# Optimization experiments

Measured on AMD Instinct MI355X. Metric: run time of the kernel, lower is better.

Reference implementation:

```python
import jax, jax.numpy as jnp
import numpy as np

B, M, L, IN_C, MID_C, OUT_C = 1, 128, 256, 256, 32, 128


def setup_inputs() -> dict:
    key = jax.random.key(0)
    k_x, k_proj, k_final = jax.random.split(key, 3)
    return {
        "x1d": jax.random.normal(k_x, (B, M, L, IN_C), dtype=jnp.float32),
        "norm_w": jnp.ones((IN_C,), dtype=jnp.float32),
        "norm_b": jnp.zeros((IN_C,), dtype=jnp.float32),
        "proj_w": jax.random.normal(k_proj, (2 * MID_C, IN_C), dtype=jnp.float32) * 0.02,
        "proj_b": jnp.zeros((2 * MID_C,), dtype=jnp.float32),
        "final_w": jax.random.normal(k_final, (OUT_C, MID_C * MID_C), dtype=jnp.float32) * 0.02,
        "final_b": jnp.zeros((OUT_C,), dtype=jnp.float32),
    }


def reference(x1d, norm_w, norm_b, proj_w, proj_b, final_w, final_b):
    # LayerNorm over channel dim
    mu = jnp.mean(x1d, axis=-1, keepdims=True)
    var = jnp.mean(jnp.square(x1d - mu), axis=-1, keepdims=True)
    x = (x1d - mu) * jax.lax.rsqrt(var + 1e-5) * norm_w + norm_b

    mid_c = proj_w.shape[0] // 2
    # Linear -> (b, m, L, 2*mid_c); view (..., mid_c, 2); chunk & squeeze:
    # i = interleaved even channels, j = interleaved odd channels
    p = jnp.einsum('bmlc,dc->bmld', x, proj_w) + proj_b
    p = p.reshape(*p.shape[:-1], mid_c, 2)
    i, j = p[..., 0], p[..., 1]          # each (b, m, L, mid_c)

    m = x1d.shape[1]
    # Outer product mean over the MSA (m) dimension -> (b, L, L, mid_c, mid_c)
    x2d = jnp.einsum('bmix,bmjy->bijxy', i, j) / m

    b, li, lj = x2d.shape[0], x2d.shape[1], x2d.shape[2]
    flat = x2d.reshape(b, li, lj, mid_c * mid_c)
    out = jnp.einsum('bijf,of->bijo', flat, final_w) + final_b
    return out
```

## Files before the change

kernel.cpp:

```cpp
#include <hip/hip_runtime.h>
#include <hip/hip_bf16.h>

#define DEVINL __device__ __forceinline__

typedef float  f32x4_t  __attribute__((ext_vector_type(4)));
typedef float  f32x16_t __attribute__((ext_vector_type(16)));
typedef short  bf16x8_t __attribute__((ext_vector_type(8)));

#define MFMA16(a,b,c) __builtin_amdgcn_mfma_f32_16x16x32_bf16((a),(b),(c),0,0,0)
#define MFMA32(a,b,c) __builtin_amdgcn_mfma_f32_32x32x16_bf16((a),(b),(c),0,0,0)

DEVINL unsigned short f2bf(float f) {
  union { float f; unsigned u; } v; v.f = f;
  unsigned r = v.u + 0x7fffu + ((v.u >> 16) & 1u);
  return (unsigned short)(r >> 16);
}

DEVINL unsigned pk2bf(float lo, float hi) {
  union { __hip_bfloat162 h2; unsigned u; } v;
  v.h2 = __float22bfloat162_rn(make_float2(lo, hi));
  return v.u;
}


__global__ __launch_bounds__(256) void kA(const float* __restrict__ x,
                                          const float* __restrict__ nw,
                                          const float* __restrict__ nb,
                                          const float* __restrict__ pw,
                                          const float* __restrict__ pb,
                                          const float* __restrict__ fw,
                                          unsigned short* __restrict__ Wb,
                                          unsigned short* __restrict__ Ig,
                                          unsigned short* __restrict__ Jg) {
  if (blockIdx.x >= 1024) {
    int T = (blockIdx.x - 1024) * 256 + threadIdx.x;
    int o     = T >> 8;
    int kpos0 = (T & 255) * 4;
    int y  = kpos0 >> 5;
    int x0 = kpos0 & 31;
    const float* fo = fw + o * 1024 + y;
    ushort4 u;
    u.x = f2bf(fo[(x0 + 0) * 32]);
    u.y = f2bf(fo[(x0 + 1) * 32]);
    u.z = f2bf(fo[(x0 + 2) * 32]);
    u.w = f2bf(fo[(x0 + 3) * 32]);
    size_t off = (size_t)((o >> 5) * 64 + (kpos0 >> 4)) * 512 + (o & 31) * 16
               + ((kpos0 >> 3) & 1) * 8 + (kpos0 & 7);
    *(ushort4*)&Wb[off] = u;
    return;
  }
  __shared__ unsigned short xnl[32 * 264];
  __shared__ unsigned short pwl[64 * 264];
  __shared__ unsigned short ep[64 * 36];
  const int tid  = threadIdx.x;
  const int wv   = tid >> 6;
  const int lane = tid & 63;
  const int q    = lane >> 4;
  const int ln16 = lane & 15;
  const int l    = blockIdx.x & 255;
  const int m0   = (blockIdx.x >> 8) * 32;

  const float4* xs = (const float4*)x;
  float4 v[8];
#pragma unroll
  for (int i = 0; i < 8; i++) {
    int row = m0 + i * 4 + wv;
    v[i] = xs[row * 16384 + l * 64 + lane];
  }
  float4 nw4 = ((const float4*)nw)[lane];
  float4 nb4 = ((const float4*)nb)[lane];

#pragma unroll
  for (int i = 0; i < 8; i++) {
    float s  = v[i].x + v[i].y + v[i].z + v[i].w;
    float ss = v[i].x * v[i].x + v[i].y * v[i].y + v[i].z * v[i].z + v[i].w * v[i].w;
#pragma unroll
    for (int off = 32; off > 0; off >>= 1) {
      s  += __shfl_xor(s, off);
      ss += __shfl_xor(ss, off);
    }
    float mu  = s * (1.0f / 256.0f);
    float var = ss * (1.0f / 256.0f) - mu * mu;
    float rs  = rsqrtf(var + 1e-5f);
    ushort4 u;
    u.x = f2bf((v[i].x - mu) * rs * nw4.x + nb4.x);
    u.y = f2bf((v[i].y - mu) * rs * nw4.y + nb4.y);
    u.z = f2bf((v[i].z - mu) * rs * nw4.z + nb4.z);
    u.w = f2bf((v[i].w - mu) * rs * nw4.w + nb4.w);
    *(ushort4*)&xnl[(i * 4 + wv) * 264 + lane * 4] = u;
  }

  const float4* ps = (const float4*)pw;
#pragma unroll
  for (int i = 0; i < 16; i++) {
    float4 w4 = ps[i * 256 + tid];
    ushort4 u;
    u.x = f2bf(w4.x); u.y = f2bf(w4.y); u.z = f2bf(w4.z); u.w = f2bf(w4.w);
    *(ushort4*)&pwl[(i * 4 + wv) * 264 + lane * 4] = u;
  }
  __syncthreads();

  const int rt = wv & 1;
  const int db = (wv >> 1) * 32;
  f32x4_t acc[2] = {{0.f, 0.f, 0.f, 0.f}, {0.f, 0.f, 0.f, 0.f}};
#pragma unroll
  for (int kc = 0; kc < 8; kc++) {
    bf16x8_t a  = *(const bf16x8_t*)&xnl[(rt * 16 + ln16) * 264 + kc * 32 + q * 8];
    bf16x8_t b0 = *(const bf16x8_t*)&pwl[(db + ln16) * 264 + kc * 32 + q * 8];
    bf16x8_t b1 = *(const bf16x8_t*)&pwl[(db + 16 + ln16) * 264 + kc * 32 + q * 8];
    acc[0] = MFMA16(a, b0, acc[0]);
    acc[1] = MFMA16(a, b1, acc[1]);
  }

#pragma unroll
  for (int t2 = 0; t2 < 2; t2++) {
    int d = db + t2 * 16 + ln16;
    float bias  = pb[d];
    float scale = (d & 1) ? 1.0f : (1.0f / 128.0f);
#pragma unroll
    for (int r = 0; r < 4; r++) {
      int mloc = rt * 16 + q * 4 + r;
      ep[d * 36 + mloc] = f2bf((acc[t2][r] + bias) * scale);
    }
  }
  __syncthreads();

  const int h  = tid >> 3;
  const int m4 = tid & 7;
  const size_t off = (size_t)(l * 8 + (m0 >> 4) + (m4 >> 2)) * 512 + h * 16 + ((m4 >> 1) & 1) * 8 + (m4 & 1) * 4;
  ushort4 vi = *(const ushort4*)&ep[(2 * h) * 36 + m4 * 4];
  *(ushort4*)&Ig[off] = vi;
  ushort4 vj = *(const ushort4*)&ep[(2 * h + 1) * 36 + m4 * 4];
  *(ushort4*)&Jg[off] = vj;
}

__global__ __launch_bounds__(512, 4) void kB(const unsigned short* __restrict__ Ig,
                                             const unsigned short* __restrict__ Jg,
                                             const unsigned short* __restrict__ Wb,
                                             const float* __restrict__ fb,
                                             float* __restrict__ out) {
  extern __shared__ unsigned short fl[];
  constexpr int P = 1048;
  const int tid  = threadIdx.x;
  const int w    = tid >> 6;
  const int lane = tid & 63;
  const int ln32 = lane & 31;
  const int h    = lane >> 5;
  const int p    = blockIdx.x >> 4;
  const int t    = blockIdx.x & 15;

  const int u  = w & 1;
  const int sq = w >> 1;
  bf16x8_t af[8];
#pragma unroll
  for (int mc = 0; mc < 8; mc++)
    af[mc] = *(const bf16x8_t*)&Ig[(size_t)((p * 2 + u) * 8 + mc) * 512 + ln32 * 16 + h * 8];

#pragma unroll
  for (int s = 0; s < 4; s++) {
    const int jl = sq * 4 + s;
    const size_t jbase = (size_t)(t * 16 + jl) * 4096 + ln32 * 16 + h * 8;
    bf16x8_t jb[8];
#pragma unroll
    for (int mc = 0; mc < 8; mc++) jb[mc] = *(const bf16x8_t*)&Jg[jbase + mc * 512];
    f32x16_t c;
#pragma unroll
    for (int i = 0; i < 16; i++) c[i] = 0.f;
#pragma unroll
    for (int mc = 0; mc < 8; mc++) c = MFMA32(af[mc], jb[mc], c);
    unsigned short* fr = &fl[(u * 16 + jl) * P];
#pragma unroll
    for (int g = 0; g < 4; g++) {
      int cp = (4 * ln32 + g) ^ (ln32 & 7);
      uint2 pv;
      pv.x = pk2bf(c[4 * g + 0], c[4 * g + 1]);
      pv.y = pk2bf(c[4 * g + 2], c[4 * g + 3]);
      *(uint2*)&fr[cp * 8 + h * 4] = pv;
    }
  }

  const int ot = w & 3;
  const int kh = w >> 2;
  const unsigned short* Wp = Wb + (size_t)(ot * 64 + kh * 32) * 512 + ln32 * 16 + h * 8;
  bf16x8_t bq[8];
  bq[0] = *(const bf16x8_t*)&Wp[0];
  bq[1] = *(const bf16x8_t*)&Wp[512];

  __syncthreads();

#pragma unroll
  for (int i = 2; i < 8; i++) bq[i] = *(const bf16x8_t*)&Wp[(size_t)i * 512];

#define LDA(kc) (*(const bf16x8_t*)&fl[ln32 * P + \
    ((((kh * 32 + (kc)) * 2 + h) ^ (((kh * 32 + (kc)) >> 1) & 7)) * 8)])

  f32x16_t o2[2];
#pragma unroll
  for (int i = 0; i < 16; i++) { o2[0][i] = 0.f; o2[1][i] = 0.f; }

  bf16x8_t aq[4];
  aq[0] = LDA(0); aq[1] = LDA(1); aq[2] = LDA(2); aq[3] = LDA(3);

#pragma unroll
  for (int kc = 0; kc < 32; kc += 2) {
    bf16x8_t ac0 = aq[kc & 3],      ac1 = aq[(kc + 1) & 3];
    bf16x8_t bc0 = bq[kc & 7],      bc1 = bq[(kc + 1) & 7];
    if (kc < 28) { aq[kc & 3] = LDA(kc + 4); aq[(kc + 1) & 3] = LDA(kc + 5); }
    if (kc < 24) {
      bq[kc & 7]       = *(const bf16x8_t*)&Wp[(size_t)(kc + 8) * 512];
      bq[(kc + 1) & 7] = *(const bf16x8_t*)&Wp[(size_t)(kc + 9) * 512];
    }
    o2[0] = MFMA32(ac0, bc0, o2[0]);
    o2[1] = MFMA32(ac1, bc1, o2[1]);
  }
#undef LDA

#pragma unroll
  for (int i = 0; i < 16; i++) o2[0][i] += o2[1][i];

  __syncthreads();
  float* red = (float*)fl;
  if (kh == 1) {
#pragma unroll
    for (int q = 0; q < 4; q++) {
      int idx = ot * 1024 + lane * 16 + ((q ^ (lane & 3)) * 4);
      *(float4*)&red[idx] = make_float4(o2[0][4 * q + 0], o2[0][4 * q + 1],
                                        o2[0][4 * q + 2], o2[0][4 * q + 3]);
    }
  }
  __syncthreads();
  if (kh == 0) {
#pragma unroll
    for (int q = 0; q < 4; q++) {
      int idx = ot * 1024 + lane * 16 + ((q ^ (lane & 3)) * 4);
      float4 rv = *(const float4*)&red[idx];
      o2[0][4 * q + 0] += rv.x; o2[0][4 * q + 1] += rv.y;
      o2[0][4 * q + 2] += rv.z; o2[0][4 * q + 3] += rv.w;
    }
    const float bias = fb[ot * 32 + ln32];
    float* ob = out + ((size_t)(p * 2) * 256 + t * 16) * 128 + ot * 32 + ln32;
#pragma unroll
    for (int r = 0; r < 16; r++) {
      int br = (r & 3) + 8 * (r >> 2) + 4 * h;
      ob[(br >> 4) * 32768 + (br & 15) * 128] = o2[0][r] + bias;
    }
  }
}

extern "C" void kernel_launch(void* const* d_in, const int* in_sizes, int n_in,
                              void* d_out, int out_size, void* d_ws, size_t ws_size,
                              hipStream_t stream) {
  const float* x1d     = (const float*)d_in[0];
  const float* norm_w  = (const float*)d_in[1];
  const float* norm_b  = (const float*)d_in[2];
  const float* proj_w  = (const float*)d_in[3];
  const float* proj_b  = (const float*)d_in[4];
  const float* final_w = (const float*)d_in[5];
  const float* final_b = (const float*)d_in[6];
  float* outp          = (float*)d_out;

  unsigned short* Wb  = (unsigned short*)d_ws;
  unsigned short* Igp = Wb + 131072;
  unsigned short* Jgp = Igp + 1048576;

  const int kb_lds = 32 * 1048 * 2;
  hipFuncSetAttribute((const void*)kB, hipFuncAttributeMaxDynamicSharedMemorySize, kb_lds);

  kA<<<1152, 256, 0, stream>>>(x1d, norm_w, norm_b, proj_w, proj_b, final_w, Wb, Igp, Jgp);
  kB<<<2048, 512, kb_lds, stream>>>(Igp, Jgp, Wb, final_b, outp);
}
```

Before: 138.8 us.

## Double kB tile to 64 output rows per 1024-thread block

```diff
diff --git a/kernel.cpp b/kernel.cpp
--- a/kernel.cpp
+++ b/kernel.cpp
@@ -134,11 +134,11 @@
   *(ushort4*)&Jg[off] = vj;
 }
 
-__global__ __launch_bounds__(512, 4) void kB(const unsigned short* __restrict__ Ig,
-                                             const unsigned short* __restrict__ Jg,
-                                             const unsigned short* __restrict__ Wb,
-                                             const float* __restrict__ fb,
-                                             float* __restrict__ out) {
+__global__ __launch_bounds__(1024, 4) void kB(const unsigned short* __restrict__ Ig,
+                                              const unsigned short* __restrict__ Jg,
+                                              const unsigned short* __restrict__ Wb,
+                                              const float* __restrict__ fb,
+                                              float* __restrict__ out) {
   extern __shared__ unsigned short fl[];
   constexpr int P = 1048;
   const int tid  = threadIdx.x;
@@ -149,101 +149,108 @@
   const int p    = blockIdx.x >> 4;
   const int t    = blockIdx.x & 15;
 
-  const int u  = w & 1;
-  const int sq = w >> 1;
-  bf16x8_t af[8];
-#pragma unroll
-  for (int mc = 0; mc < 8; mc++)
-    af[mc] = *(const bf16x8_t*)&Ig[(size_t)((p * 2 + u) * 8 + mc) * 512 + ln32 * 16 + h * 8];
-
-#pragma unroll
-  for (int s = 0; s < 4; s++) {
-    const int jl = sq * 4 + s;
-    const size_t jbase = (size_t)(t * 16 + jl) * 4096 + ln32 * 16 + h * 8;
-    bf16x8_t jb[8];
-#pragma unroll
-    for (int mc = 0; mc < 8; mc++) jb[mc] = *(const bf16x8_t*)&Jg[jbase + mc * 512];
-    f32x16_t c;
-#pragma unroll
-    for (int i = 0; i < 16; i++) c[i] = 0.f;
-#pragma unroll
-    for (int mc = 0; mc < 8; mc++) c = MFMA32(af[mc], jb[mc], c);
-    unsigned short* fr = &fl[(u * 16 + jl) * P];
-#pragma unroll
-    for (int g = 0; g < 4; g++) {
-      int cp = (4 * ln32 + g) ^ (ln32 & 7);
-      uint2 pv;
-      pv.x = pk2bf(c[4 * g + 0], c[4 * g + 1]);
-      pv.y = pk2bf(c[4 * g + 2], c[4 * g + 3]);
-      *(uint2*)&fr[cp * 8 + h * 4] = pv;
+  {
+    const int il = w & 3;
+    const int sq = w >> 2;
+    bf16x8_t af[8];
+#pragma unroll
+    for (int mc = 0; mc < 8; mc++)
+      af[mc] = *(const bf16x8_t*)&Ig[(size_t)((p * 4 + il) * 8 + mc) * 512 + ln32 * 16 + h * 8];
+
+#pragma unroll
+    for (int s = 0; s < 4; s++) {
+      const int jl = sq * 4 + s;
+      const size_t jbase = (size_t)(t * 16 + jl) * 4096 + ln32 * 16 + h * 8;
+      bf16x8_t jb[8];
+#pragma unroll
+      for (int mc = 0; mc < 8; mc++) jb[mc] = *(const bf16x8_t*)&Jg[jbase + mc * 512];
+      f32x16_t c;
+#pragma unroll
+      for (int i = 0; i < 16; i++) c[i] = 0.f;
+#pragma unroll
+      for (int mc = 0; mc < 8; mc++) c = MFMA32(af[mc], jb[mc], c);
+      unsigned short* fr = &fl[(il * 16 + jl) * P];
+#pragma unroll
+      for (int g = 0; g < 4; g++) {
+        int cp = (4 * ln32 + g) ^ (ln32 & 7);
+        uint2 pv;
+        pv.x = pk2bf(c[4 * g + 0], c[4 * g + 1]);
+        pv.y = pk2bf(c[4 * g + 2], c[4 * g + 3]);
+        *(uint2*)&fr[cp * 8 + h * 4] = pv;
+      }
     }
   }
 
   const int ot = w & 3;
-  const int kh = w >> 2;
-  const unsigned short* Wp = Wb + (size_t)(ot * 64 + kh * 32) * 512 + ln32 * 16 + h * 8;
-  bf16x8_t bq[8];
+  const int kq = w >> 2;
+  const unsigned short* Wp = Wb + (size_t)(ot * 64 + kq * 16) * 512 + ln32 * 16 + h * 8;
+  bf16x8_t bq[4];
   bq[0] = *(const bf16x8_t*)&Wp[0];
   bq[1] = *(const bf16x8_t*)&Wp[512];
 
   __syncthreads();
 
-#pragma unroll
-  for (int i = 2; i < 8; i++) bq[i] = *(const bf16x8_t*)&Wp[(size_t)i * 512];
-
-#define LDA(kc) (*(const bf16x8_t*)&fl[ln32 * P + \
-    ((((kh * 32 + (kc)) * 2 + h) ^ (((kh * 32 + (kc)) >> 1) & 7)) * 8)])
+  bq[2] = *(const bf16x8_t*)&Wp[2 * 512];
+  bq[3] = *(const bf16x8_t*)&Wp[3 * 512];
+
+#define LDA(rt, kc) (*(const bf16x8_t*)&fl[((rt) * 32 + ln32) * P + \
+    ((((kq * 16 + (kc)) * 2 + h) ^ (((kq * 16 + (kc)) >> 1) & 7)) * 8)])
 
   f32x16_t o2[2];
 #pragma unroll
   for (int i = 0; i < 16; i++) { o2[0][i] = 0.f; o2[1][i] = 0.f; }
 
   bf16x8_t aq[4];
-  aq[0] = LDA(0); aq[1] = LDA(1); aq[2] = LDA(2); aq[3] = LDA(3);
-
-#pragma unroll
-  for (int kc = 0; kc < 32; kc += 2) {
-    bf16x8_t ac0 = aq[kc & 3],      ac1 = aq[(kc + 1) & 3];
-    bf16x8_t bc0 = bq[kc & 7],      bc1 = bq[(kc + 1) & 7];
-    if (kc < 28) { aq[kc & 3] = LDA(kc + 4); aq[(kc + 1) & 3] = LDA(kc + 5); }
-    if (kc < 24) {
-      bq[kc & 7]       = *(const bf16x8_t*)&Wp[(size_t)(kc + 8) * 512];
-      bq[(kc + 1) & 7] = *(const bf16x8_t*)&Wp[(size_t)(kc + 9) * 512];
-    }
-    o2[0] = MFMA32(ac0, bc0, o2[0]);
-    o2[1] = MFMA32(ac1, bc1, o2[1]);
+  aq[0] = LDA(0, 0); aq[1] = LDA(1, 0);
+  aq[2] = LDA(0, 1); aq[3] = LDA(1, 1);
+
+#pragma unroll
+  for (int kc = 0; kc < 16; kc++) {
+    const int sl = (kc & 1) * 2;
+    bf16x8_t a0 = aq[sl], a1 = aq[sl + 1];
+    bf16x8_t bc = bq[kc & 3];
+    if (kc < 14) { aq[sl] = LDA(0, kc + 2); aq[sl + 1] = LDA(1, kc + 2); }
+    if (kc < 12) bq[kc & 3] = *(const bf16x8_t*)&Wp[(size_t)(kc + 4) * 512];
+    o2[0] = MFMA32(a0, bc, o2[0]);
+    o2[1] = MFMA32(a1, bc, o2[1]);
   }
 #undef LDA
 
-#pragma unroll
-  for (int i = 0; i < 16; i++) o2[0][i] += o2[1][i];
-
   __syncthreads();
   float* red = (float*)fl;
-  if (kh == 1) {
-#pragma unroll
-    for (int q = 0; q < 4; q++) {
-      int idx = ot * 1024 + lane * 16 + ((q ^ (lane & 3)) * 4);
-      *(float4*)&red[idx] = make_float4(o2[0][4 * q + 0], o2[0][4 * q + 1],
-                                        o2[0][4 * q + 2], o2[0][4 * q + 3]);
-    }
-  }
-  __syncthreads();
-  if (kh == 0) {
-#pragma unroll
-    for (int q = 0; q < 4; q++) {
-      int idx = ot * 1024 + lane * 16 + ((q ^ (lane & 3)) * 4);
-      float4 rv = *(const float4*)&red[idx];
-      o2[0][4 * q + 0] += rv.x; o2[0][4 * q + 1] += rv.y;
-      o2[0][4 * q + 2] += rv.z; o2[0][4 * q + 3] += rv.w;
+  if (kq != 0) {
+    const int base = (((kq - 1) * 4 + ot) * 2) * 1024;
+#pragma unroll
+    for (int rt = 0; rt < 2; rt++)
+#pragma unroll
+      for (int g = 0; g < 4; g++)
+        *(float4*)&red[base + rt * 1024 + g * 256 + lane * 4] =
+            make_float4(o2[rt][4 * g + 0], o2[rt][4 * g + 1],
+                        o2[rt][4 * g + 2], o2[rt][4 * g + 3]);
+  }
+  __syncthreads();
+  if (kq == 0) {
+#pragma unroll
+    for (int s3 = 0; s3 < 3; s3++) {
+      const int base = ((s3 * 4 + ot) * 2) * 1024;
+#pragma unroll
+      for (int rt = 0; rt < 2; rt++)
+#pragma unroll
+        for (int g = 0; g < 4; g++) {
+          float4 rv = *(const float4*)&red[base + rt * 1024 + g * 256 + lane * 4];
+          o2[rt][4 * g + 0] += rv.x; o2[rt][4 * g + 1] += rv.y;
+          o2[rt][4 * g + 2] += rv.z; o2[rt][4 * g + 3] += rv.w;
+        }
     }
     const float bias = fb[ot * 32 + ln32];
-    float* ob = out + ((size_t)(p * 2) * 256 + t * 16) * 128 + ot * 32 + ln32;
-#pragma unroll
-    for (int r = 0; r < 16; r++) {
-      int br = (r & 3) + 8 * (r >> 2) + 4 * h;
-      ob[(br >> 4) * 32768 + (br & 15) * 128] = o2[0][r] + bias;
-    }
+    float* ob = out + (size_t)(p * 4) * 32768 + t * 2048 + ot * 32 + ln32;
+#pragma unroll
+    for (int rt = 0; rt < 2; rt++)
+#pragma unroll
+      for (int r = 0; r < 16; r++) {
+        int br = rt * 32 + (r & 3) + 8 * (r >> 2) + 4 * h;
+        ob[(br >> 4) * 32768 + (br & 15) * 128] = o2[rt][r] + bias;
+      }
   }
 }
 
@@ -263,9 +270,9 @@
   unsigned short* Igp = Wb + 131072;
   unsigned short* Jgp = Igp + 1048576;
 
-  const int kb_lds = 32 * 1048 * 2;
+  const int kb_lds = 64 * 1048 * 2;
   hipFuncSetAttribute((const void*)kB, hipFuncAttributeMaxDynamicSharedMemorySize, kb_lds);
 
   kA<<<1152, 256, 0, stream>>>(x1d, norm_w, norm_b, proj_w, proj_b, final_w, Wb, Igp, Jgp);
-  kB<<<2048, 512, kb_lds, stream>>>(Igp, Jgp, Wb, final_b, outp);
-}
+  kB<<<1024, 1024, kb_lds, stream>>>(Igp, Jgp, Wb, final_b, outp);
+}
```

New measurement: 139.1 us. No clear change (+0.2%).
